# Kernel tuning notes

Hardware: AMD Instinct MI355X
Metric: run time of the kernel (lower is better)

## Reference

```python
import jax, jax.numpy as jnp
import numpy as np

B, L, H, E = 4, 2048, 8, 64
WINDOW = 8
DILATION = 1


def setup_inputs() -> dict:
    key = jax.random.key(0)
    kq, kk, kv, ka = jax.random.split(key, 4)
    queries = jax.random.normal(kq, (B, L, H, E), dtype=jnp.float32)
    keys = jax.random.normal(kk, (B, L, H, E), dtype=jnp.float32)
    values = jax.random.normal(kv, (B, L, H, E), dtype=jnp.float32)
    alpha = jax.random.uniform(ka, (1,), dtype=jnp.float32)
    return {"queries": queries, "keys": keys, "values": values, "alpha": alpha}


def _full_attention(q, k, v, scale):
    # q,k,v: [B, L, H, E]
    scores = jnp.einsum('blhe,bshe->bhls', q, k) * scale  # [B,H,L,L]
    A = jax.nn.softmax(scores, axis=-1)
    return jnp.einsum('bhls,bshd->blhd', A, v)


def _local_attention(q, k, v, scale):
    # efficient gather-based local window attention, non-causal
    Lk = k.shape[1]
    offsets = jnp.arange(-WINDOW, WINDOW + 1) * DILATION
    idx = jnp.clip(jnp.arange(Lk)[:, None] + offsets[None, :], 0, Lk - 1)
    K_win = k[:, idx]
    V_win = v[:, idx]
    scores = jnp.einsum('blhe,blwhe->blhw', q, K_win) * scale
    A = jax.nn.softmax(scores, axis=-1)
    return jnp.einsum('blhw,blwhe->blhe', A, V_win)


def reference(queries, keys, values, alpha):
    scale = 1.0 / np.sqrt(queries.shape[-1]).astype(np.float32)
    out_full = _full_attention(queries, keys, values, scale)
    out_local = _local_attention(queries, keys, values, scale)
    w = jax.nn.sigmoid(alpha[0])
    # only_target_first=True: positions 1..L-1 take out_full, position 0 is gated
    out = out_full.at[:, 0].set(w * out_full[:, 0] + (1.0 - w) * out_local[:, 0])
    return out
```

## Files before the change

kernel.cpp:

```cpp
#include <hip/hip_runtime.h>

typedef unsigned short u16;
typedef unsigned int   u32;
typedef __attribute__((ext_vector_type(8))) short short8;
typedef __attribute__((ext_vector_type(16))) float f32x16;

#define MFMA32(a, b, c) __builtin_amdgcn_mfma_f32_32x32x16_bf16(a, b, c, 0, 0, 0)

constexpr int Lv = 2048, Hv = 8, Ev = 64, HE = Hv * Ev;
constexpr float QSCALE = 0.18033688011112042f;

__device__ __forceinline__ float bf2f(u16 u) {
    u32 x = ((u32)u) << 16;
    return __builtin_bit_cast(float, x);
}
__device__ __forceinline__ u16 f2bf(float f) {
    u32 x = __builtin_bit_cast(u32, f);
    u32 r = ((x >> 16) & 1u) + 0x7fffu;
    return (u16)((x + r) >> 16);
}
__device__ __forceinline__ u32 pkbf(float a, float b) {
#if __has_builtin(__builtin_amdgcn_cvt_pk_bf16_f32)
    typedef __attribute__((ext_vector_type(2))) __bf16 bf16x2;
    bf16x2 v = __builtin_amdgcn_cvt_pk_bf16_f32(a, b);
    return __builtin_bit_cast(u32, v);
#else
    return (u32)f2bf(a) | ((u32)f2bf(b) << 16);
#endif
}
__device__ __forceinline__ float fexp2(float x) {
#if __has_builtin(__builtin_amdgcn_exp2f)
    return __builtin_amdgcn_exp2f(x);
#else
    return exp2f(x);
#endif
}

__device__ __forceinline__ int detect_isbf16(const u32* q32, int lane) {
    u32 w0 = q32[2 * lane];
    u32 w1 = q32[2 * lane + 1];
    u16 uu[4] = { (u16)(w0 & 0xffff), (u16)(w0 >> 16),
                  (u16)(w1 & 0xffff), (u16)(w1 >> 16) };
    int p = 0, z = 0;
#pragma unroll
    for (int j = 0; j < 4; ++j) {
        u16 mgn = (u16)(uu[j] & 0x7fff);
        int ex  = mgn >> 7;
        bool zero = (mgn == 0);
        bool pl   = zero || (ex >= 115 && ex <= 132);
        p += pl ? 1 : 0;
        if ((j & 1) == 0) z += zero ? 1 : 0;
    }
    int acc = p | (z << 16);
#pragma unroll
    for (int o = 1; o < 64; o <<= 1) acc += __shfl_xor(acc, o);
    int ps = acc & 0xffff, zs = acc >> 16;
    if (zs >= 100) return 0;
    return (ps >= 240) ? 1 : 0;
}

__device__ __forceinline__ short8 cvt8s(const float* p, float s) {
    float4 a = *(const float4*)p, b4 = *(const float4*)(p + 4);
    u32 r[4] = { pkbf(a.x * s, a.y * s), pkbf(a.z * s, a.w * s),
                 pkbf(b4.x * s, b4.y * s), pkbf(b4.z * s, b4.w * s) };
    return *(short8*)r;
}

__device__ __forceinline__ f32x16 zv16() {
    f32x16 z;
#pragma unroll
    for (int r = 0; r < 16; ++r) z[r] = 0.f;
    return z;
}

__device__ __forceinline__ void plswap(u32& a, u32& b) {
#if __has_builtin(__builtin_amdgcn_permlane32_swap)
    auto r = __builtin_amdgcn_permlane32_swap(a, b, false, false);
    a = r[0]; b = r[1];
#else
    int lane = (int)(threadIdx.x & 63);
    u32 ax = (u32)__shfl_xor((int)a, 32);
    u32 bx = (u32)__shfl_xor((int)b, 32);
    bool hi = lane >= 32;
    u32 na = hi ? bx : a;
    u32 nb = hi ? b  : ax;
    a = na; b = nb;
#endif
}

template <int ISBF>
__device__ __forceinline__ void attn_impl(
    const void* __restrict__ qv, const void* __restrict__ kv,
    const void* __restrict__ vv, const void* __restrict__ alphav,
    void* __restrict__ outv, u16* SMEM)
{
    const int tid  = threadIdx.x;
    const int w    = tid >> 6;
    const int lane = tid & 63;
    const int l31  = lane & 31;
    const int hi   = lane >> 5;
    const int qg   = w & 3;
    const int g    = w >> 2;

    const int fid = blockIdx.x;
    const int bh  = (fid & 7) * 4 + ((fid >> 3) & 3);
    const int rb  = fid >> 5;
    const int b   = bh >> 3, h = bh & 7;
    const int row0 = rb * 128;

    const size_t bhoff = (size_t)b * Lv * HE + h * Ev;
    const u16*   q16 = (const u16*)qv + bhoff;
    const u16*   k16 = (const u16*)kv + bhoff;
    const u16*   v16 = (const u16*)vv + bhoff;
    const float* q32 = (const float*)qv + bhoff;
    const float* k32 = (const float*)kv + bhoff;
    const float* v32 = (const float*)vv + bhoff;

    u16* Klds = SMEM;
    u16* Vt   = SMEM + 8192;

    short8 qf[4];
    {
        size_t ro = (size_t)(row0 + qg * 32 + l31) * HE + hi * 8;
        if (ISBF) {
#pragma unroll
            for (int c = 0; c < 4; ++c) {
                short8 t = *(const short8*)(q16 + ro + 16 * c);
#pragma unroll
                for (int j = 0; j < 8; ++j)
                    qf[c][j] = (short)f2bf(bf2f((u16)t[j]) * QSCALE);
            }
        } else {
#pragma unroll
            for (int c = 0; c < 4; ++c) qf[c] = cvt8s(q32 + ro + 16 * c, QSCALE);
        }
    }

    f32x16 O[2];
    O[0] = zv16(); O[1] = zv16();
    float psum = 0.f;

    const int kkey = tid >> 3, ksl = tid & 7;
    const int koff = kkey * HE + ((ksl ^ (kkey & 7)) * 8);
    const int eq = tid & 15, pp = tid >> 4;
    const int kcv = pp >> 2, pq = pp & 3;

    float4 kfa, kfb, vfa, vfb;
    uint4  kru; uint2 vru0, vru1;

#define LOAD_TILE(KT)                                                          \
    do {                                                                       \
        size_t kb_ = (size_t)(KT) * 64 * HE;                                   \
        if (ISBF) {                                                            \
            kru  = *(const uint4*)(k16 + kb_ + koff);                          \
            const u16* vp_ = v16 + kb_ + (size_t)(2 * pp) * HE + eq * 4;       \
            vru0 = *(const uint2*)vp_;                                         \
            vru1 = *(const uint2*)(vp_ + HE);                                  \
        } else {                                                               \
            const float* kp_ = k32 + kb_ + koff;                               \
            kfa = *(const float4*)kp_;                                         \
            kfb = *(const float4*)(kp_ + 4);                                   \
            const float* vp_ = v32 + kb_ + (size_t)(2 * pp) * HE + eq * 4;     \
            vfa = *(const float4*)vp_;                                         \
            vfb = *(const float4*)(vp_ + HE);                                  \
        }                                                                      \
    } while (0)

#define STORE_TILE(KB, VB)                                                     \
    do {                                                                       \
        if (ISBF) {                                                            \
            *(uint4*)&(KB)[tid * 8] = kru;                                     \
            const u16* a0_ = (const u16*)&vru0;                                \
            const u16* a1_ = (const u16*)&vru1;                                \
            _Pragma("unroll")                                                  \
            for (int j = 0; j < 4; ++j) {                                      \
                int e_  = eq * 4 + j;                                          \
                int sl_ = kcv ^ ((e_ + (e_ >> 3)) & 7);                        \
                u32 val_ = (u32)a0_[j] | ((u32)a1_[j] << 16);                  \
                *(u32*)&(VB)[e_ * 64 + sl_ * 8 + pq * 2] = val_;               \
            }                                                                  \
        } else {                                                               \
            u32 kk_[4] = { pkbf(kfa.x, kfa.y), pkbf(kfa.z, kfa.w),             \
                           pkbf(kfb.x, kfb.y), pkbf(kfb.z, kfb.w) };           \
            *(uint4*)&(KB)[tid * 8] = *(uint4*)kk_;                            \
            float t0_[4] = {vfa.x, vfa.y, vfa.z, vfa.w};                       \
            float t1_[4] = {vfb.x, vfb.y, vfb.z, vfb.w};                       \
            _Pragma("unroll")                                                  \
            for (int j = 0; j < 4; ++j) {                                      \
                int e_  = eq * 4 + j;                                          \
                int sl_ = kcv ^ ((e_ + (e_ >> 3)) & 7);                        \
                *(u32*)&(VB)[e_ * 64 + sl_ * 8 + pq * 2] = pkbf(t0_[j], t1_[j]);\
            }                                                                  \
        }                                                                      \
    } while (0)

    LOAD_TILE(0);
    STORE_TILE(Klds, Vt);
    __syncthreads();

    for (int kt = 0; kt < 32; ++kt) {
        u16* Kb = Klds + (kt & 1) * 4096;
        u16* Vb = Vt   + (kt & 1) * 4096;
        u16* Kn = Klds + ((kt & 1) ^ 1) * 4096;
        u16* Vn = Vt   + ((kt & 1) ^ 1) * 4096;

        if (kt < 31) LOAD_TILE(kt + 1);

        f32x16 St = zv16();
#pragma unroll
        for (int c = 0; c < 4; ++c) {
            int sl = (2 * c + hi) ^ (l31 & 7);
            short8 kf = *(const short8*)&Kb[(g * 32 + l31) * 64 + sl * 8];
            St = MFMA32(kf, qf[c], St);
        }

        float pe[16];
#pragma unroll
        for (int r = 0; r < 16; ++r) pe[r] = fexp2(St[r]);
#pragma unroll
        for (int r = 0; r < 16; ++r) psum += pe[r];
        u32 c8[8];
#pragma unroll
        for (int q = 0; q < 8; ++q) c8[q] = pkbf(pe[2 * q], pe[2 * q + 1]);
#pragma unroll
        for (int t = 0; t < 2; ++t) {
            u32 a0 = c8[4 * t + 0], a1 = c8[4 * t + 1];
            u32 a2 = c8[4 * t + 2], a3 = c8[4 * t + 3];
            plswap(a0, a2);
            plswap(a1, a3);
            u32 pw_[4] = { a0, a1, a2, a3 };
            short8 pa = *(short8*)pw_;
            int ks = 2 * g + t;
#pragma unroll
            for (int et = 0; et < 2; ++et) {
                int e  = et * 32 + l31;
                int sl = (2 * ks + hi) ^ ((e + (e >> 3)) & 7);
                short8 vf = *(const short8*)&Vb[e * 64 + sl * 8];
                O[et] = MFMA32(pa, vf, O[et]);
            }
        }

        if (kt < 31) {
            STORE_TILE(Kn, Vn);
            __syncthreads();
        }
    }
#undef LOAD_TILE
#undef STORE_TILE

    __syncthreads();
    float pst = psum + __shfl_xor(psum, 32);
    float* cb = (float*)SMEM;
    const int cbase = qg * 2368 + lane * 36;

    if (g == 1) {
        union { f32x16 v; float4 q4[4]; } u;
        u.v = O[0];
#pragma unroll
        for (int i = 0; i < 4; ++i) *(float4*)&cb[cbase + 4 * i] = u.q4[i];
        u.v = O[1];
#pragma unroll
        for (int i = 0; i < 4; ++i) *(float4*)&cb[cbase + 16 + 4 * i] = u.q4[i];
        cb[qg * 2368 + 2304 + lane] = pst;
    }

    float locv[2] = {0.f, 0.f};
    float wgt = 0.f;
    const bool w0blk = (rb == 0) && (w == 0);
    if (w0blk) {
        const int e = lane;
        const size_t base = bhoff + e;
#define LDIN(p, i) (ISBF ? bf2f(((const u16*)(p))[i]) : ((const float*)(p))[i])
        float qe = LDIN(qv, base);
        float s[9];
#pragma unroll
        for (int j = 0; j < 9; ++j) {
            float prod = qe * LDIN(kv, base + (size_t)j * HE);
#pragma unroll
            for (int o = 1; o < 64; o <<= 1) prod += __shfl_xor(prod, o);
            s[j] = prod * 0.125f;
        }
        float mx = s[0];
#pragma unroll
        for (int j = 1; j < 9; ++j) mx = fmaxf(mx, s[j]);
        float we[9];
#pragma unroll
        for (int j = 0; j < 9; ++j) we[j] = expf(s[j] - mx);
        float denom = 9.f * we[0];
        float acc   = 9.f * we[0] * LDIN(vv, base);
#pragma unroll
        for (int j = 1; j < 9; ++j) {
            denom += we[j];
            acc   += we[j] * LDIN(vv, base + (size_t)j * HE);
        }
        float loc = acc / denom;

        float a;
        if (ISBF) {
            a = bf2f(((const u16*)alphav)[0]);
            if (!(a >= 0.0f && a <= 1.0f)) {
                float af = ((const float*)alphav)[0];
                if (af >= 0.0f && af <= 1.0f) a = af;
            }
        } else {
            a = ((const float*)alphav)[0];
            if (!(a >= 0.0f && a <= 1.0f)) {
                float ab = bf2f(((const u16*)alphav)[0]);
                if (ab >= 0.0f && ab <= 1.0f) a = ab;
            }
        }
        wgt = 1.f / (1.f + expf(-a));
#pragma unroll
        for (int et = 0; et < 2; ++et) locv[et] = __shfl(loc, et * 32 + l31);
#undef LDIN
    }

    __syncthreads();
    if (g != 0) return;

    float pstp = cb[qg * 2368 + 2304 + lane];
#pragma unroll
    for (int r = 0; r < 16; ++r) {
        O[0][r] += cb[cbase + r];
        O[1][r] += cb[cbase + 16 + r];
    }
    float invv = 1.0f / (pst + pstp);

#pragma unroll
    for (int rg = 0; rg < 4; ++rg) {
#pragma unroll
        for (int rr = 0; rr < 4; ++rr) {
            const int reg = rg * 4 + rr;
            const int rl  = rr + 8 * rg + 4 * hi;
            float inv = __shfl(invv, rl);
            int row = row0 + qg * 32 + rl;
            size_t oo = (size_t)(b * Lv + row) * HE + h * Ev + l31;
            bool blend = w0blk && (rl == 0);
#pragma unroll
            for (int et = 0; et < 2; ++et) {
                float res = O[et][reg] * inv;
                if (blend) res = wgt * res + (1.f - wgt) * locv[et];
                if (ISBF) ((u16*)outv)[oo + et * 32] = f2bf(res);
                else      ((float*)outv)[oo + et * 32] = res;
            }
        }
    }
}

__global__ __launch_bounds__(512, 4) void attn_kernel(
    const void* __restrict__ qv, const void* __restrict__ kv,
    const void* __restrict__ vv, const void* __restrict__ alphav,
    void* __restrict__ outv)
{
    __shared__ u16 SMEM[18944];

    const int isbf = detect_isbf16((const u32*)qv, threadIdx.x & 63);
    if (isbf) attn_impl<1>(qv, kv, vv, alphav, outv, SMEM);
    else      attn_impl<0>(qv, kv, vv, alphav, outv, SMEM);
}

extern "C" void kernel_launch(void* const* d_in, const int* in_sizes, int n_in,
                              void* d_out, int out_size, void* d_ws, size_t ws_size,
                              hipStream_t stream) {
    hipLaunchKernelGGL(attn_kernel, dim3(512), dim3(512), 0, stream,
                       d_in[0], d_in[1], d_in[2], d_in[3], d_out);
}
```

Measured before the change: 146.5 us.

## Double key tile size to 128 per iteration and add MFMA priority hints

The key/value tile per loop iteration grows from 64 to 128 rows, so the loop runs 16 times instead of 32 and each wave computes two 32x32 score blocks with independent MFMA chains. This halves the number of barriers and gives more independent work between global loads and LDS stores. Shared memory per block rises to 64KB, which may lower occupancy below the launch-bounds target of 4 blocks. s_setprio hints are also wrapped around the MFMA sections.

```diff
diff --git a/kernel.cpp b/kernel.cpp
--- a/kernel.cpp
+++ b/kernel.cpp
@@ -117,7 +117,7 @@
     const float* v32 = (const float*)vv + bhoff;
 
     u16* Klds = SMEM;
-    u16* Vt   = SMEM + 8192;
+    u16* Vt   = SMEM + 16384;
 
     short8 qf[4];
     {
@@ -143,110 +143,142 @@
     const int kkey = tid >> 3, ksl = tid & 7;
     const int koff = kkey * HE + ((ksl ^ (kkey & 7)) * 8);
     const int eq = tid & 15, pp = tid >> 4;
-    const int kcv = pp >> 2, pq = pp & 3;
-
-    float4 kfa, kfb, vfa, vfb;
-    uint4  kru; uint2 vru0, vru1;
+    const int s8a = pp >> 2, pq = pp & 3;
+
+    float4 kfa, kfb, kfc, kfd, vfa, vfb, vfc, vfd;
+    uint4  kru0, kru1; uint2 vru0, vru1, vru2, vru3;
 
 #define LOAD_TILE(KT)                                                          \
     do {                                                                       \
-        size_t kb_ = (size_t)(KT) * 64 * HE;                                   \
+        size_t kb_ = (size_t)(KT) * 128 * HE;                                  \
         if (ISBF) {                                                            \
-            kru  = *(const uint4*)(k16 + kb_ + koff);                          \
-            const u16* vp_ = v16 + kb_ + (size_t)(2 * pp) * HE + eq * 4;       \
-            vru0 = *(const uint2*)vp_;                                         \
-            vru1 = *(const uint2*)(vp_ + HE);                                  \
+            kru0 = *(const uint4*)(k16 + kb_ + koff);                          \
+            kru1 = *(const uint4*)(k16 + kb_ + koff + 64 * HE);                \
+            const u16* vp0_ = v16 + kb_ + (size_t)(2 * pp) * HE + eq * 4;      \
+            vru0 = *(const uint2*)vp0_;                                        \
+            vru1 = *(const uint2*)(vp0_ + HE);                                 \
+            vru2 = *(const uint2*)(vp0_ + 64 * HE);                            \
+            vru3 = *(const uint2*)(vp0_ + 65 * HE);                            \
         } else {                                                               \
             const float* kp_ = k32 + kb_ + koff;                               \
             kfa = *(const float4*)kp_;                                         \
             kfb = *(const float4*)(kp_ + 4);                                   \
-            const float* vp_ = v32 + kb_ + (size_t)(2 * pp) * HE + eq * 4;     \
-            vfa = *(const float4*)vp_;                                         \
-            vfb = *(const float4*)(vp_ + HE);                                  \
+            kfc = *(const float4*)(kp_ + 64 * HE);                             \
+            kfd = *(const float4*)(kp_ + 64 * HE + 4);                         \
+            const float* vp0_ = v32 + kb_ + (size_t)(2 * pp) * HE + eq * 4;    \
+            vfa = *(const float4*)vp0_;                                        \
+            vfb = *(const float4*)(vp0_ + HE);                                 \
+            vfc = *(const float4*)(vp0_ + 64 * HE);                            \
+            vfd = *(const float4*)(vp0_ + 65 * HE);                            \
         }                                                                      \
     } while (0)
 
 #define STORE_TILE(KB, VB)                                                     \
     do {                                                                       \
         if (ISBF) {                                                            \
-            *(uint4*)&(KB)[tid * 8] = kru;                                     \
+            *(uint4*)&(KB)[tid * 8]         = kru0;                            \
+            *(uint4*)&(KB)[(tid + 512) * 8] = kru1;                            \
             const u16* a0_ = (const u16*)&vru0;                                \
             const u16* a1_ = (const u16*)&vru1;                                \
+            const u16* a2_ = (const u16*)&vru2;                                \
+            const u16* a3_ = (const u16*)&vru3;                                \
             _Pragma("unroll")                                                  \
             for (int j = 0; j < 4; ++j) {                                      \
                 int e_  = eq * 4 + j;                                          \
-                int sl_ = kcv ^ ((e_ + (e_ >> 3)) & 7);                        \
-                u32 val_ = (u32)a0_[j] | ((u32)a1_[j] << 16);                  \
-                *(u32*)&(VB)[e_ * 64 + sl_ * 8 + pq * 2] = val_;               \
+                int sl_ = s8a ^ ((e_ + (e_ >> 3)) & 7);                        \
+                int ad_ = e_ * 128 + sl_ * 8 + pq * 2;                         \
+                *(u32*)&(VB)[ad_]      = (u32)a0_[j] | ((u32)a1_[j] << 16);    \
+                *(u32*)&(VB)[ad_ + 64] = (u32)a2_[j] | ((u32)a3_[j] << 16);    \
             }                                                                  \
         } else {                                                               \
-            u32 kk_[4] = { pkbf(kfa.x, kfa.y), pkbf(kfa.z, kfa.w),             \
+            u32 k0_[4] = { pkbf(kfa.x, kfa.y), pkbf(kfa.z, kfa.w),             \
                            pkbf(kfb.x, kfb.y), pkbf(kfb.z, kfb.w) };           \
-            *(uint4*)&(KB)[tid * 8] = *(uint4*)kk_;                            \
+            u32 k1_[4] = { pkbf(kfc.x, kfc.y), pkbf(kfc.z, kfc.w),             \
+                           pkbf(kfd.x, kfd.y), pkbf(kfd.z, kfd.w) };           \
+            *(uint4*)&(KB)[tid * 8]         = *(uint4*)k0_;                    \
+            *(uint4*)&(KB)[(tid + 512) * 8] = *(uint4*)k1_;                    \
             float t0_[4] = {vfa.x, vfa.y, vfa.z, vfa.w};                       \
             float t1_[4] = {vfb.x, vfb.y, vfb.z, vfb.w};                       \
+            float t2_[4] = {vfc.x, vfc.y, vfc.z, vfc.w};                       \
+            float t3_[4] = {vfd.x, vfd.y, vfd.z, vfd.w};                       \
             _Pragma("unroll")                                                  \
             for (int j = 0; j < 4; ++j) {                                      \
                 int e_  = eq * 4 + j;                                          \
-                int sl_ = kcv ^ ((e_ + (e_ >> 3)) & 7);                        \
-                *(u32*)&(VB)[e_ * 64 + sl_ * 8 + pq * 2] = pkbf(t0_[j], t1_[j]);\
+                int sl_ = s8a ^ ((e_ + (e_ >> 3)) & 7);                        \
+                int ad_ = e_ * 128 + sl_ * 8 + pq * 2;                         \
+                *(u32*)&(VB)[ad_]      = pkbf(t0_[j], t1_[j]);                 \
+                *(u32*)&(VB)[ad_ + 64] = pkbf(t2_[j], t3_[j]);                 \
             }                                                                  \
         }                                                                      \
     } while (0)
 
+#define SMPV(STX, CK)                                                          \
+    do {                                                                       \
+        float pe[16];                                                          \
+        _Pragma("unroll")                                                      \
+        for (int r = 0; r < 16; ++r) { pe[r] = fexp2((STX)[r]); }              \
+        _Pragma("unroll")                                                      \
+        for (int r = 0; r < 16; ++r) psum += pe[r];                            \
+        u32 c8[8];                                                             \
+        _Pragma("unroll")                                                      \
+        for (int q = 0; q < 8; ++q) c8[q] = pkbf(pe[2 * q], pe[2 * q + 1]);    \
+        _Pragma("unroll")                                                      \
+        for (int t = 0; t < 2; ++t) {                                          \
+            u32 a0 = c8[4 * t + 0], a1 = c8[4 * t + 1];                        \
+            u32 a2 = c8[4 * t + 2], a3 = c8[4 * t + 3];                        \
+            plswap(a0, a2);                                                    \
+            plswap(a1, a3);                                                    \
+            u32 pw_[4] = { a0, a1, a2, a3 };                                   \
+            short8 pa = *(short8*)pw_;                                         \
+            int ks = 4 * g + 2 * (CK) + t;                                     \
+            __builtin_amdgcn_s_setprio(1);                                     \
+            _Pragma("unroll")                                                  \
+            for (int et = 0; et < 2; ++et) {                                   \
+                int e   = et * 32 + l31;                                       \
+                int s8r = 2 * ks + hi;                                         \
+                int sl  = (s8r & 8) | ((s8r & 7) ^ ((e + (e >> 3)) & 7));      \
+                short8 vf = *(const short8*)&Vb[e * 128 + sl * 8];             \
+                O[et] = MFMA32(pa, vf, O[et]);                                 \
+            }                                                                  \
+            __builtin_amdgcn_s_setprio(0);                                     \
+        }                                                                      \
+    } while (0)
+
     LOAD_TILE(0);
     STORE_TILE(Klds, Vt);
     __syncthreads();
 
-    for (int kt = 0; kt < 32; ++kt) {
-        u16* Kb = Klds + (kt & 1) * 4096;
-        u16* Vb = Vt   + (kt & 1) * 4096;
-        u16* Kn = Klds + ((kt & 1) ^ 1) * 4096;
-        u16* Vn = Vt   + ((kt & 1) ^ 1) * 4096;
-
-        if (kt < 31) LOAD_TILE(kt + 1);
-
-        f32x16 St = zv16();
+    for (int kt = 0; kt < 16; ++kt) {
+        u16* Kb = Klds + (kt & 1) * 8192;
+        u16* Vb = Vt   + (kt & 1) * 8192;
+        u16* Kn = Klds + ((kt & 1) ^ 1) * 8192;
+        u16* Vn = Vt   + ((kt & 1) ^ 1) * 8192;
+
+        if (kt < 15) LOAD_TILE(kt + 1);
+
+        f32x16 St0 = zv16(), St1 = zv16();
+        __builtin_amdgcn_s_setprio(1);
 #pragma unroll
         for (int c = 0; c < 4; ++c) {
             int sl = (2 * c + hi) ^ (l31 & 7);
-            short8 kf = *(const short8*)&Kb[(g * 32 + l31) * 64 + sl * 8];
-            St = MFMA32(kf, qf[c], St);
-        }
-
-        float pe[16];
-#pragma unroll
-        for (int r = 0; r < 16; ++r) pe[r] = fexp2(St[r]);
-#pragma unroll
-        for (int r = 0; r < 16; ++r) psum += pe[r];
-        u32 c8[8];
-#pragma unroll
-        for (int q = 0; q < 8; ++q) c8[q] = pkbf(pe[2 * q], pe[2 * q + 1]);
-#pragma unroll
-        for (int t = 0; t < 2; ++t) {
-            u32 a0 = c8[4 * t + 0], a1 = c8[4 * t + 1];
-            u32 a2 = c8[4 * t + 2], a3 = c8[4 * t + 3];
-            plswap(a0, a2);
-            plswap(a1, a3);
-            u32 pw_[4] = { a0, a1, a2, a3 };
-            short8 pa = *(short8*)pw_;
-            int ks = 2 * g + t;
-#pragma unroll
-            for (int et = 0; et < 2; ++et) {
-                int e  = et * 32 + l31;
-                int sl = (2 * ks + hi) ^ ((e + (e >> 3)) & 7);
-                short8 vf = *(const short8*)&Vb[e * 64 + sl * 8];
-                O[et] = MFMA32(pa, vf, O[et]);
-            }
-        }
-
-        if (kt < 31) {
+            short8 kf0 = *(const short8*)&Kb[(g * 64 + l31) * 64 + sl * 8];
+            short8 kf1 = *(const short8*)&Kb[(g * 64 + 32 + l31) * 64 + sl * 8];
+            St0 = MFMA32(kf0, qf[c], St0);
+            St1 = MFMA32(kf1, qf[c], St1);
+        }
+        __builtin_amdgcn_s_setprio(0);
+
+        SMPV(St0, 0);
+        SMPV(St1, 1);
+
+        if (kt < 15) {
             STORE_TILE(Kn, Vn);
             __syncthreads();
         }
     }
 #undef LOAD_TILE
 #undef STORE_TILE
+#undef SMPV
 
     __syncthreads();
     float pst = psum + __shfl_xor(psum, 32);
@@ -352,7 +384,7 @@
     const void* __restrict__ vv, const void* __restrict__ alphav,
     void* __restrict__ outv)
 {
-    __shared__ u16 SMEM[18944];
+    __shared__ u16 SMEM[32768];
 
     const int isbf = detect_isbf16((const u32*)qv, threadIdx.x & 63);
     if (isbf) attn_impl<1>(qv, kv, vv, alphav, outv, SMEM);
```

After: 190.7 us. +30.2%, slower.

## Deepen K/V register prefetch to two tiles ahead with MFMA priority hints

Applied to the files above, without the earlier changes.

Global loads of K/V now run two tiles ahead, using two ping-pong register sets (A/B) and a loop unrolled by two, so each load has a full extra iteration to land before its LDS store. The __syncthreads is replaced by an explicit lgkmcnt wait plus s_barrier, which drops the wait on outstanding global loads. s_setprio raises wave priority around the MFMA blocks. The cost is higher register pressure from the doubled staging registers, which could lower occupancy.

```diff
diff --git a/kernel.cpp b/kernel.cpp
--- a/kernel.cpp
+++ b/kernel.cpp
@@ -145,33 +145,33 @@
     const int eq = tid & 15, pp = tid >> 4;
     const int kcv = pp >> 2, pq = pp & 3;
 
-    float4 kfa, kfb, vfa, vfb;
-    uint4  kru; uint2 vru0, vru1;
-
-#define LOAD_TILE(KT)                                                          \
+    float4 kfaA, kfbA, vfaA, vfbA, kfaB, kfbB, vfaB, vfbB;
+    uint4  kruA, kruB; uint2 vru0A, vru1A, vru0B, vru1B;
+
+#define LOAD_TILE(S, KT)                                                       \
     do {                                                                       \
         size_t kb_ = (size_t)(KT) * 64 * HE;                                   \
         if (ISBF) {                                                            \
-            kru  = *(const uint4*)(k16 + kb_ + koff);                          \
+            kru##S  = *(const uint4*)(k16 + kb_ + koff);                       \
             const u16* vp_ = v16 + kb_ + (size_t)(2 * pp) * HE + eq * 4;       \
-            vru0 = *(const uint2*)vp_;                                         \
-            vru1 = *(const uint2*)(vp_ + HE);                                  \
+            vru0##S = *(const uint2*)vp_;                                      \
+            vru1##S = *(const uint2*)(vp_ + HE);                               \
         } else {                                                               \
             const float* kp_ = k32 + kb_ + koff;                               \
-            kfa = *(const float4*)kp_;                                         \
-            kfb = *(const float4*)(kp_ + 4);                                   \
+            kfa##S = *(const float4*)kp_;                                      \
+            kfb##S = *(const float4*)(kp_ + 4);                                \
             const float* vp_ = v32 + kb_ + (size_t)(2 * pp) * HE + eq * 4;     \
-            vfa = *(const float4*)vp_;                                         \
-            vfb = *(const float4*)(vp_ + HE);                                  \
+            vfa##S = *(const float4*)vp_;                                      \
+            vfb##S = *(const float4*)(vp_ + HE);                               \
         }                                                                      \
     } while (0)
 
-#define STORE_TILE(KB, VB)                                                     \
+#define STORE_TILE(S, KB, VB)                                                  \
     do {                                                                       \
         if (ISBF) {                                                            \
-            *(uint4*)&(KB)[tid * 8] = kru;                                     \
-            const u16* a0_ = (const u16*)&vru0;                                \
-            const u16* a1_ = (const u16*)&vru1;                                \
+            *(uint4*)&(KB)[tid * 8] = kru##S;                                  \
+            const u16* a0_ = (const u16*)&vru0##S;                             \
+            const u16* a1_ = (const u16*)&vru1##S;                             \
             _Pragma("unroll")                                                  \
             for (int j = 0; j < 4; ++j) {                                      \
                 int e_  = eq * 4 + j;                                          \
@@ -180,11 +180,11 @@
                 *(u32*)&(VB)[e_ * 64 + sl_ * 8 + pq * 2] = val_;               \
             }                                                                  \
         } else {                                                               \
-            u32 kk_[4] = { pkbf(kfa.x, kfa.y), pkbf(kfa.z, kfa.w),             \
-                           pkbf(kfb.x, kfb.y), pkbf(kfb.z, kfb.w) };           \
+            u32 kk_[4] = { pkbf(kfa##S.x, kfa##S.y), pkbf(kfa##S.z, kfa##S.w), \
+                           pkbf(kfb##S.x, kfb##S.y), pkbf(kfb##S.z, kfb##S.w) };\
             *(uint4*)&(KB)[tid * 8] = *(uint4*)kk_;                            \
-            float t0_[4] = {vfa.x, vfa.y, vfa.z, vfa.w};                       \
-            float t1_[4] = {vfb.x, vfb.y, vfb.z, vfb.w};                       \
+            float t0_[4] = {vfa##S.x, vfa##S.y, vfa##S.z, vfa##S.w};           \
+            float t1_[4] = {vfb##S.x, vfb##S.y, vfb##S.z, vfb##S.w};           \
             _Pragma("unroll")                                                  \
             for (int j = 0; j < 4; ++j) {                                      \
                 int e_  = eq * 4 + j;                                          \
@@ -194,59 +194,70 @@
         }                                                                      \
     } while (0)
 
-    LOAD_TILE(0);
-    STORE_TILE(Klds, Vt);
-    __syncthreads();
-
-    for (int kt = 0; kt < 32; ++kt) {
-        u16* Kb = Klds + (kt & 1) * 4096;
-        u16* Vb = Vt   + (kt & 1) * 4096;
-        u16* Kn = Klds + ((kt & 1) ^ 1) * 4096;
-        u16* Vn = Vt   + ((kt & 1) ^ 1) * 4096;
-
-        if (kt < 31) LOAD_TILE(kt + 1);
-
-        f32x16 St = zv16();
-#pragma unroll
-        for (int c = 0; c < 4; ++c) {
-            int sl = (2 * c + hi) ^ (l31 & 7);
-            short8 kf = *(const short8*)&Kb[(g * 32 + l31) * 64 + sl * 8];
-            St = MFMA32(kf, qf[c], St);
-        }
-
-        float pe[16];
-#pragma unroll
-        for (int r = 0; r < 16; ++r) pe[r] = fexp2(St[r]);
-#pragma unroll
-        for (int r = 0; r < 16; ++r) psum += pe[r];
-        u32 c8[8];
-#pragma unroll
-        for (int q = 0; q < 8; ++q) c8[q] = pkbf(pe[2 * q], pe[2 * q + 1]);
-#pragma unroll
-        for (int t = 0; t < 2; ++t) {
-            u32 a0 = c8[4 * t + 0], a1 = c8[4 * t + 1];
-            u32 a2 = c8[4 * t + 2], a3 = c8[4 * t + 3];
-            plswap(a0, a2);
-            plswap(a1, a3);
-            u32 pw_[4] = { a0, a1, a2, a3 };
-            short8 pa = *(short8*)pw_;
-            int ks = 2 * g + t;
-#pragma unroll
-            for (int et = 0; et < 2; ++et) {
-                int e  = et * 32 + l31;
-                int sl = (2 * ks + hi) ^ ((e + (e >> 3)) & 7);
-                short8 vf = *(const short8*)&Vb[e * 64 + sl * 8];
-                O[et] = MFMA32(pa, vf, O[et]);
-            }
-        }
-
-        if (kt < 31) {
-            STORE_TILE(Kn, Vn);
-            __syncthreads();
-        }
+#define BODY(KT, SL, SS)                                                       \
+    do {                                                                       \
+        u16* Kb = Klds + ((KT) & 1) * 4096;                                    \
+        u16* Vb = Vt   + ((KT) & 1) * 4096;                                    \
+        if ((KT) < 30) LOAD_TILE(SL, (KT) + 2);                                \
+        f32x16 St = zv16();                                                    \
+        __builtin_amdgcn_s_setprio(1);                                         \
+        _Pragma("unroll")                                                      \
+        for (int c = 0; c < 4; ++c) {                                          \
+            int sl = (2 * c + hi) ^ (l31 & 7);                                 \
+            short8 kf = *(const short8*)&Kb[(g * 32 + l31) * 64 + sl * 8];     \
+            St = MFMA32(kf, qf[c], St);                                        \
+        }                                                                      \
+        __builtin_amdgcn_s_setprio(0);                                         \
+        float pe[16];                                                          \
+        _Pragma("unroll")                                                      \
+        for (int r = 0; r < 16; ++r) pe[r] = fexp2(St[r]);                     \
+        _Pragma("unroll")                                                      \
+        for (int r = 0; r < 16; ++r) psum += pe[r];                            \
+        u32 c8[8];                                                             \
+        _Pragma("unroll")                                                      \
+        for (int q = 0; q < 8; ++q) c8[q] = pkbf(pe[2 * q], pe[2 * q + 1]);    \
+        _Pragma("unroll")                                                      \
+        for (int t = 0; t < 2; ++t) {                                          \
+            u32 a0 = c8[4 * t + 0], a1 = c8[4 * t + 1];                        \
+            u32 a2 = c8[4 * t + 2], a3 = c8[4 * t + 3];                        \
+            plswap(a0, a2);                                                    \
+            plswap(a1, a3);                                                    \
+            u32 pw_[4] = { a0, a1, a2, a3 };                                   \
+            short8 pa = *(short8*)pw_;                                         \
+            int ks = 2 * g + t;                                                \
+            __builtin_amdgcn_s_setprio(1);                                     \
+            _Pragma("unroll")                                                  \
+            for (int et = 0; et < 2; ++et) {                                   \
+                int e  = et * 32 + l31;                                        \
+                int sl = (2 * ks + hi) ^ ((e + (e >> 3)) & 7);                 \
+                short8 vf = *(const short8*)&Vb[e * 64 + sl * 8];              \
+                O[et] = MFMA32(pa, vf, O[et]);                                 \
+            }                                                                  \
+            __builtin_amdgcn_s_setprio(0);                                     \
+        }                                                                      \
+        if ((KT) < 31) {                                                       \
+            u16* Kn = Klds + (((KT) + 1) & 1) * 4096;                          \
+            u16* Vn = Vt   + (((KT) + 1) & 1) * 4096;                          \
+            STORE_TILE(SS, Kn, Vn);                                            \
+            asm volatile("s_waitcnt lgkmcnt(0)" ::: "memory");                 \
+            __builtin_amdgcn_s_barrier();                                      \
+        }                                                                      \
+    } while (0)
+
+    LOAD_TILE(A, 0);
+    LOAD_TILE(B, 1);
+    STORE_TILE(A, Klds, Vt);
+    asm volatile("s_waitcnt lgkmcnt(0)" ::: "memory");
+    __builtin_amdgcn_s_barrier();
+
+    for (int kt2 = 0; kt2 < 16; ++kt2) {
+        const int kt = 2 * kt2;
+        BODY(kt,     A, B);
+        BODY(kt + 1, B, A);
     }
 #undef LOAD_TILE
 #undef STORE_TILE
+#undef BODY
 
     __syncthreads();
     float pst = psum + __shfl_xor(psum, 32);
```

New measurement: 144.1 us. Within noise of the previous version (-1.6%).
